# Kernel tuning notes

Hardware: AMD Instinct MI355X
Metric: run time of the kernel (lower is better)

## Reference

```python
import jax, jax.numpy as jnp
import numpy as np
import math

L, D, H, FF = 12, 768, 12, 3072
DH = D // H
REL_BINS, MAX_REL = 32, 128
REL2D_BINS, MAX_REL2D = 64, 256
EPS = 1e-5
ALPHA = 32.0


def rel_bucket(rp, num_buckets, max_distance):
    # bidirectional T5-style bucketing, matches relative_position_bucket
    nb = num_buckets // 2
    ret = (rp > 0).astype(jnp.int32) * nb
    n = jnp.abs(rp)
    max_exact = nb // 2
    is_small = n < max_exact
    val_if_large = max_exact + (
        jnp.log(jnp.maximum(n, 1).astype(jnp.float32) / max_exact)
        / math.log(max_distance / max_exact) * (nb - max_exact)
    ).astype(jnp.int32)
    val_if_large = jnp.minimum(val_if_large, nb - 1)
    return ret + jnp.where(is_small, n.astype(jnp.int32), val_if_large)


def layernorm(x, g, b):
    mu = jnp.mean(x, axis=-1, keepdims=True)
    var = jnp.mean(jnp.square(x - mu), axis=-1, keepdims=True)
    return (x - mu) * jax.lax.rsqrt(var + EPS) * g + b


def cogview_softmax(scores):
    # PB-Relax stabilized softmax
    ss = scores / ALPHA
    m = jnp.max(ss, axis=-1, keepdims=True)
    return jax.nn.softmax((ss - m) * ALPHA, axis=-1)


def setup_inputs() -> dict:
    key = jax.random.key(0)
    ks = jax.random.split(key, 24)
    B, S = 4, 512
    s = 0.02
    inp = {
        'hidden_states': jax.random.normal(ks[0], (B, S, D), jnp.float32),
        'attention_mask': jnp.zeros((B, 1, 1, S), jnp.float32),
        'position_ids': jnp.arange(B * S, dtype=jnp.int64).reshape(B, S),
        'bbox': jax.random.randint(ks[1], (B, S, 4), 0, 1000, jnp.int64),
        'Wq': jax.random.normal(ks[2], (L, D, D)) * s,
        'bq': jnp.zeros((L, D)),
        'Wk': jax.random.normal(ks[3], (L, D, D)) * s,
        'bk': jnp.zeros((L, D)),
        'Wv': jax.random.normal(ks[4], (L, D, D)) * s,
        'bv': jnp.zeros((L, D)),
        'Wo': jax.random.normal(ks[5], (L, D, D)) * s,
        'bo': jnp.zeros((L, D)),
        'ln1_g': jnp.ones((L, D)),
        'ln1_b': jnp.zeros((L, D)),
        'Wi': jax.random.normal(ks[6], (L, D, FF)) * s,
        'bi': jnp.zeros((L, FF)),
        'Wo2': jax.random.normal(ks[7], (L, FF, D)) * s,
        'bo2': jnp.zeros((L, D)),
        'ln2_g': jnp.ones((L, D)),
        'ln2_b': jnp.zeros((L, D)),
        'rel_w': jax.random.normal(ks[8], (REL_BINS, H)) * s,   # rel_pos_bias.weight.T
        'relx_w': jax.random.normal(ks[9], (REL2D_BINS, H)) * s,
        'rely_w': jax.random.normal(ks[10], (REL2D_BINS, H)) * s,
    }
    return inp


def encoder_forward(hidden_states, attention_mask, position_ids, bbox,
                    Wq, bq, Wk, bk, Wv, bv, Wo, bo, ln1_g, ln1_b,
                    Wi, bi, Wo2, bo2, ln2_g, ln2_b, rel_w, relx_w, rely_w):
    B, S, _ = hidden_states.shape
    inv_sqrt = 1.0 / math.sqrt(DH)

    # 1D relative position bias: [B,H,S,S]
    rp = position_ids[:, None, :] - position_ids[:, :, None]  # [B,S,S]
    b1 = rel_bucket(rp, REL_BINS, MAX_REL)
    rel_pos = jnp.transpose(rel_w[b1], (0, 3, 1, 2))

    # 2D spatial bias from bbox x (coord 0) and y (coord 3)
    px = bbox[:, :, 0]
    py = bbox[:, :, 3]
    bx = rel_bucket(px[:, None, :] - px[:, :, None], REL2D_BINS, MAX_REL2D)
    by = rel_bucket(py[:, None, :] - py[:, :, None], REL2D_BINS, MAX_REL2D)
    rel_2d_pos = jnp.transpose(relx_w[bx], (0, 3, 1, 2)) + jnp.transpose(rely_w[by], (0, 3, 1, 2))

    bias = (rel_pos + rel_2d_pos) * inv_sqrt + attention_mask  # [B,H,S,S]

    x = hidden_states
    for i in range(L):
        q = (x @ Wq[i] + bq[i]).reshape(B, S, H, DH).transpose(0, 2, 1, 3)
        k = (x @ Wk[i] + bk[i]).reshape(B, S, H, DH).transpose(0, 2, 1, 3)
        v = (x @ Wv[i] + bv[i]).reshape(B, S, H, DH).transpose(0, 2, 1, 3)
        scores = jnp.einsum('bhqd,bhkd->bhqk', q * inv_sqrt, k) + bias
        probs = cogview_softmax(scores)
        ctx = jnp.einsum('bhqk,bhkd->bhqd', probs, v)
        ctx = ctx.transpose(0, 2, 1, 3).reshape(B, S, D)
        attn_out = layernorm(ctx @ Wo[i] + bo[i] + x, ln1_g[i], ln1_b[i])
        h = jax.nn.gelu(attn_out @ Wi[i] + bi[i], approximate=False)
        x = layernorm(h @ Wo2[i] + bo2[i] + attn_out, ln2_g[i], ln2_b[i])
    return x


def reference(hidden_states, attention_mask, position_ids, bbox,
              Wq, bq, Wk, bk, Wv, bv, Wo, bo, ln1_g, ln1_b,
              Wi, bi, Wo2, bo2, ln2_g, ln2_b, rel_w, relx_w, rely_w):
    return encoder_forward(hidden_states, attention_mask, position_ids, bbox,
                           Wq, bq, Wk, bk, Wv, bv, Wo, bo, ln1_g, ln1_b,
                           Wi, bi, Wo2, bo2, ln2_g, ln2_b, rel_w, relx_w, rely_w)
```

## Files before the change

### kernel.cpp

```cpp
#include <hip/hip_runtime.h>
#include <hip/hip_bf16.h>


typedef __attribute__((ext_vector_type(8))) short short8;
typedef __attribute__((ext_vector_type(4))) float f32x4;
typedef __attribute__((ext_vector_type(4))) unsigned int u32x4;
typedef __attribute__((ext_vector_type(4))) unsigned short us4;

#define DEVI static __device__ __forceinline__

DEVI unsigned short f2bf(float f) {
  union { float f; unsigned u; } x; x.f = f;
  unsigned u = x.u;
  u += 0x7fffu + ((u >> 16) & 1u);
  return (unsigned short)(u >> 16);
}
DEVI float bf2f(unsigned short h) {
  union { unsigned u; float f; } x; x.u = ((unsigned)h) << 16;
  return x.f;
}
DEVI int xcd_swz(int bid, int nwg) {
  int q = nwg >> 3, r = nwg & 7;
  int x = bid & 7, o = bid >> 3;
  return (x < r ? x * (q + 1) : r * (q + 1) + (x - r) * q) + o;
}

DEVI void gemm64(const unsigned short* __restrict__ A, int lda,
                 const float* __restrict__ W, int ldw, int K,
                 int m0, f32x4 acc[4], char* lds) {
  const int tid = threadIdx.x;
  const int l = tid & 63, w = tid >> 6;
  const int n_st = tid & 63;
  const int kb = (tid >> 6) << 4;
  const unsigned short* Ar = A + (size_t)(m0 + 16 * w + (l & 15)) * lda + ((l >> 4) << 3);
  for (int kt = 0; kt < K; kt += 64) {
    float f[16];
#pragma unroll
    for (int j = 0; j < 16; ++j)
      f[j] = W[(size_t)(kt + kb + j) * ldw + n_st];
    __syncthreads();
#pragma unroll
    for (int c = 0; c < 2; ++c) {
      u32x4 p;
#pragma unroll
      for (int q2 = 0; q2 < 4; ++q2)
        p[q2] = (unsigned)f2bf(f[c * 8 + q2 * 2]) | ((unsigned)f2bf(f[c * 8 + q2 * 2 + 1]) << 16);
      int koff = (kb + c * 8) << 1;
      int addr = (n_st << 7) + (koff ^ ((n_st & 7) << 4));
      *(u32x4*)(lds + addr) = p;
    }
    __syncthreads();
#pragma unroll
    for (int ks = 0; ks < 2; ++ks) {
      short8 a = *(const short8*)(Ar + kt + ks * 32);
#pragma unroll
      for (int fb = 0; fb < 4; ++fb) {
        int nn = (fb << 4) + (l & 15);
        int koff = (ks * 32 + ((l >> 4) << 3)) << 1;
        int addr = (nn << 7) + (koff ^ ((nn & 7) << 4));
        short8 b = *(const short8*)(lds + addr);
        acc[fb] = __builtin_amdgcn_mfma_f32_16x16x32_bf16(a, b, acc[fb], 0, 0, 0);
      }
    }
  }
}

__global__ __launch_bounds__(256) void k_qkv(
    const unsigned short* __restrict__ xb,
    const float* __restrict__ Wq, const float* __restrict__ Wk, const float* __restrict__ Wv,
    const float* __restrict__ bq, const float* __restrict__ bk, const float* __restrict__ bv,
    unsigned short* __restrict__ q_out, unsigned short* __restrict__ k_out,
    unsigned short* __restrict__ vT_out, int layer) {
  __shared__ u32x4 lds4[512];
  char* lds = (char*)lds4;
  const int wid = xcd_swz(blockIdx.x, gridDim.x);
  const int bm = wid % 32, bn = wid / 32;
  const int which = bn / 12;
  const int nloc = (bn % 12) * 64;
  const float* W = (which == 0 ? Wq : which == 1 ? Wk : Wv) + (size_t)layer * 589824 + nloc;
  const float* bias = (which == 0 ? bq : which == 1 ? bk : bv) + layer * 768 + nloc;
  f32x4 acc[4];
#pragma unroll
  for (int i = 0; i < 4; ++i) acc[i] = (f32x4){0.f, 0.f, 0.f, 0.f};
  gemm64(xb, 768, W, 768, 768, bm * 64, acc, lds);
  const int tid = threadIdx.x, l = tid & 63, w = tid >> 6;
  const int h = nloc >> 6;
  const int r0 = bm * 64 + 16 * w + ((l >> 4) << 2);
  const int batch = r0 >> 9, s0 = r0 & 511;
  const int bh = batch * 12 + h;
  const float scale = (which == 0) ? 0.125f : 1.0f;
#pragma unroll
  for (int fb = 0; fb < 4; ++fb) {
    const int c = (fb << 4) + (l & 15);
    const float bv_ = bias[c];
    if (which == 2) {
      us4 pk;
#pragma unroll
      for (int j = 0; j < 4; ++j) pk[j] = f2bf(acc[fb][j] + bv_);
      *(us4*)(vT_out + ((size_t)bh * 64 + c) * 512 + s0) = pk;
    } else {
      unsigned short* dst = (which == 0 ? q_out : k_out);
#pragma unroll
      for (int j = 0; j < 4; ++j)
        dst[((size_t)bh * 512 + s0 + j) * 64 + c] = f2bf((acc[fb][j] + bv_) * scale);
    }
  }
}

__global__ __launch_bounds__(256) void k_attn(
    const unsigned short* __restrict__ qb, const unsigned short* __restrict__ kb,
    const unsigned short* __restrict__ biasb, unsigned short* __restrict__ probs) {
  const int bh = blockIdx.y;
  const int q0 = blockIdx.x * 64;
  const int tid = threadIdx.x, l = tid & 63, w = tid >> 6;
  const unsigned short* Q = qb + ((size_t)bh * 512 + q0 + 16 * w + (l & 15)) * 64 + ((l >> 4) << 3);
  const unsigned short* Kp = kb + (size_t)bh * 32768 + (size_t)(l & 15) * 64 + ((l >> 4) << 3);
  f32x4 acc[32];
#pragma unroll
  for (int i = 0; i < 32; ++i) acc[i] = (f32x4){0.f, 0.f, 0.f, 0.f};
#pragma unroll
  for (int ks = 0; ks < 2; ++ks) {
    short8 a = *(const short8*)(Q + ks * 32);
#pragma unroll
    for (int f = 0; f < 32; ++f) {
      short8 b = *(const short8*)(Kp + (size_t)f * 1024 + ks * 32);
      acc[f] = __builtin_amdgcn_mfma_f32_16x16x32_bf16(a, b, acc[f], 0, 0, 0);
    }
  }
  const int r0 = q0 + 16 * w + ((l >> 4) << 2);
  const unsigned short* Brow = biasb + ((size_t)bh * 512 + r0) * 512 + (l & 15);
  unsigned short* Prow = probs + ((size_t)bh * 512 + r0) * 512 + (l & 15);
#pragma unroll
  for (int j = 0; j < 4; ++j) {
    float m = -3.0e38f;
#pragma unroll
    for (int f = 0; f < 32; ++f) {
      float v = acc[f][j] + bf2f(Brow[(size_t)j * 512 + (f << 4)]);
      acc[f][j] = v;
      m = fmaxf(m, v);
    }
#pragma unroll
    for (int off = 1; off < 16; off <<= 1) m = fmaxf(m, __shfl_xor(m, off));
    float s = 0.f;
#pragma unroll
    for (int f = 0; f < 32; ++f) {
      float e = __expf(acc[f][j] - m);
      acc[f][j] = e;
      s += e;
    }
#pragma unroll
    for (int off = 1; off < 16; off <<= 1) s += __shfl_xor(s, off);
    const float inv = 1.0f / s;
#pragma unroll
    for (int f = 0; f < 32; ++f)
      Prow[(size_t)j * 512 + (f << 4)] = f2bf(acc[f][j] * inv);
  }
}

__global__ __launch_bounds__(256) void k_pv(
    const unsigned short* __restrict__ probs, const unsigned short* __restrict__ vT,
    unsigned short* __restrict__ ctx) {
  const int bh = blockIdx.y;
  const int q0 = blockIdx.x * 64;
  const int tid = threadIdx.x, l = tid & 63, w = tid >> 6;
  const unsigned short* Ar = probs + ((size_t)bh * 512 + q0 + 16 * w + (l & 15)) * 512 + ((l >> 4) << 3);
  const unsigned short* Vb = vT + (size_t)bh * 32768 + (size_t)(l & 15) * 512 + ((l >> 4) << 3);
  f32x4 acc[4];
#pragma unroll
  for (int i = 0; i < 4; ++i) acc[i] = (f32x4){0.f, 0.f, 0.f, 0.f};
#pragma unroll 4
  for (int kt = 0; kt < 512; kt += 32) {
    short8 a = *(const short8*)(Ar + kt);
#pragma unroll
    for (int f = 0; f < 4; ++f) {
      short8 b = *(const short8*)(Vb + (size_t)f * 8192 + kt);
      acc[f] = __builtin_amdgcn_mfma_f32_16x16x32_bf16(a, b, acc[f], 0, 0, 0);
    }
  }
  const int batch = bh / 12, h = bh % 12;
  const int r0 = q0 + 16 * w + ((l >> 4) << 2);
#pragma unroll
  for (int fb = 0; fb < 4; ++fb) {
    const int c = (fb << 4) + (l & 15);
#pragma unroll
    for (int j = 0; j < 4; ++j)
      ctx[((size_t)(batch * 512 + r0 + j)) * 768 + h * 64 + c] = f2bf(acc[fb][j]);
  }
}

__global__ __launch_bounds__(256) void k_gemm_bias(
    const unsigned short* __restrict__ A, int lda, int K,
    const float* __restrict__ W, int ldw,
    const float* __restrict__ bias, float* __restrict__ outf, int N, int nbm) {
  __shared__ u32x4 lds4[512];
  char* lds = (char*)lds4;
  const int wid = xcd_swz(blockIdx.x, gridDim.x);
  const int bm = wid % nbm, bn = wid / nbm;
  f32x4 acc[4];
#pragma unroll
  for (int i = 0; i < 4; ++i) acc[i] = (f32x4){0.f, 0.f, 0.f, 0.f};
  gemm64(A, lda, W + bn * 64, ldw, K, bm * 64, acc, lds);
  const int tid = threadIdx.x, l = tid & 63, w = tid >> 6;
  const int r0 = bm * 64 + 16 * w + ((l >> 4) << 2);
  const int c0 = bn * 64;
#pragma unroll
  for (int fb = 0; fb < 4; ++fb) {
    const int c = c0 + (fb << 4) + (l & 15);
    const float bb = bias[c];
#pragma unroll
    for (int j = 0; j < 4; ++j)
      outf[(size_t)(r0 + j) * N + c] = acc[fb][j] + bb;
  }
}

__global__ __launch_bounds__(256) void k_gemm_gelu(
    const unsigned short* __restrict__ A, int lda, int K,
    const float* __restrict__ W, int ldw,
    const float* __restrict__ bias, unsigned short* __restrict__ outb, int N, int nbm) {
  __shared__ u32x4 lds4[512];
  char* lds = (char*)lds4;
  const int wid = xcd_swz(blockIdx.x, gridDim.x);
  const int bm = wid % nbm, bn = wid / nbm;
  f32x4 acc[4];
#pragma unroll
  for (int i = 0; i < 4; ++i) acc[i] = (f32x4){0.f, 0.f, 0.f, 0.f};
  gemm64(A, lda, W + bn * 64, ldw, K, bm * 64, acc, lds);
  const int tid = threadIdx.x, l = tid & 63, w = tid >> 6;
  const int r0 = bm * 64 + 16 * w + ((l >> 4) << 2);
  const int c0 = bn * 64;
#pragma unroll
  for (int fb = 0; fb < 4; ++fb) {
    const int c = c0 + (fb << 4) + (l & 15);
    const float bb = bias[c];
#pragma unroll
    for (int j = 0; j < 4; ++j) {
      float v = acc[fb][j] + bb;
      v = 0.5f * v * (1.0f + erff(v * 0.70710678118654752f));
      outb[(size_t)(r0 + j) * N + c] = f2bf(v);
    }
  }
}

__global__ __launch_bounds__(256) void k_ln(
    const float* __restrict__ x, const float* __restrict__ res,
    const float* __restrict__ g, const float* __restrict__ bb,
    float* __restrict__ outf, unsigned short* __restrict__ outb) {
  const int row = blockIdx.x, tid = threadIdx.x;
  const float* X = x + (size_t)row * 768;
  const float* R = res + (size_t)row * 768;
  float v[3];
  float s = 0.f;
#pragma unroll
  for (int i = 0; i < 3; ++i) { v[i] = X[tid + (i << 8)] + R[tid + (i << 8)]; s += v[i]; }
  __shared__ float red[4];
#pragma unroll
  for (int off = 32; off; off >>= 1) s += __shfl_xor(s, off);
  if ((tid & 63) == 0) red[tid >> 6] = s;
  __syncthreads();
  const float mu = (red[0] + red[1] + red[2] + red[3]) * (1.f / 768.f);
  float s2 = 0.f;
#pragma unroll
  for (int i = 0; i < 3; ++i) { float d = v[i] - mu; s2 += d * d; }
  __syncthreads();
#pragma unroll
  for (int off = 32; off; off >>= 1) s2 += __shfl_xor(s2, off);
  if ((tid & 63) == 0) red[tid >> 6] = s2;
  __syncthreads();
  const float rstd = rsqrtf((red[0] + red[1] + red[2] + red[3]) * (1.f / 768.f) + 1e-5f);
#pragma unroll
  for (int i = 0; i < 3; ++i) {
    const int c = tid + (i << 8);
    const float o = (v[i] - mu) * rstd * g[c] + bb[c];
    outf[(size_t)row * 768 + c] = o;
    outb[(size_t)row * 768 + c] = f2bf(o);
  }
}

__global__ __launch_bounds__(256) void k_init(const float* __restrict__ h,
                                              float* __restrict__ xf,
                                              unsigned short* __restrict__ xb, int n) {
  int i = blockIdx.x * 256 + threadIdx.x;
  if (i < n) { float v = h[i]; xf[i] = v; xb[i] = f2bf(v); }
}

DEVI int rbucket(int rp, int nb, int mex) {
  int ret = rp > 0 ? nb : 0;
  int n = rp < 0 ? -rp : rp;
  if (n < mex) return ret + n;
  float v = logf((float)n / (float)mex) * 0.36067376022224085f * (float)(nb - mex);
  int vi = mex + (int)v;
  vi = vi < (nb - 1) ? vi : (nb - 1);
  return ret + vi;
}

__global__ __launch_bounds__(256) void k_bias(
    const int* __restrict__ pos, const int* __restrict__ bbox,
    const float* __restrict__ mask,
    const float* __restrict__ rel_w, const float* __restrict__ relx_w,
    const float* __restrict__ rely_w, unsigned short* __restrict__ biasb) {
  __shared__ float tw[1920];
  for (int i = threadIdx.x; i < 1920; i += 256)
    tw[i] = i < 384 ? rel_w[i] : (i < 1152 ? relx_w[i - 384] : rely_w[i - 1152]);
  __syncthreads();
  const int blk = blockIdx.x;
  const int b = blk >> 9, qi = blk & 511;
  const int pi = pos[(b << 9) + qi];
  const int pxi = bbox[(((b << 9) + qi) << 2) + 0];
  const int pyi = bbox[(((b << 9) + qi) << 2) + 3];
  for (int j = threadIdx.x; j < 512; j += 256) {
    const int idx = (b << 9) + j;
    const int b1 = rbucket(pos[idx] - pi, 16, 8);
    const int bx = rbucket(bbox[(idx << 2) + 0] - pxi, 32, 16);
    const int by = rbucket(bbox[(idx << 2) + 3] - pyi, 32, 16);
    const float mk = mask[idx];
    const float* r1 = tw + b1 * 12;
    const float* r2 = tw + 384 + bx * 12;
    const float* r3 = tw + 1152 + by * 12;
#pragma unroll
    for (int h = 0; h < 12; ++h) {
      float v = (r1[h] + r2[h] + r3[h]) * 0.125f + mk;
      biasb[(((size_t)(b * 12 + h) * 512) + qi) * 512 + j] = f2bf(v);
    }
  }
}

extern "C" void kernel_launch(void* const* d_in, const int* in_sizes, int n_in,
                              void* d_out, int out_size, void* d_ws, size_t ws_size,
                              hipStream_t stream) {
  const float* hid  = (const float*)d_in[0];
  const float* mask = (const float*)d_in[1];
  const int*   pos  = (const int*)d_in[2];
  const int*   bbx  = (const int*)d_in[3];
  const float* Wq = (const float*)d_in[4];  const float* bq = (const float*)d_in[5];
  const float* Wk = (const float*)d_in[6];  const float* bk = (const float*)d_in[7];
  const float* Wv = (const float*)d_in[8];  const float* bv = (const float*)d_in[9];
  const float* Wo = (const float*)d_in[10]; const float* bo = (const float*)d_in[11];
  const float* g1 = (const float*)d_in[12]; const float* be1 = (const float*)d_in[13];
  const float* Wi = (const float*)d_in[14]; const float* bi = (const float*)d_in[15];
  const float* W2 = (const float*)d_in[16]; const float* b2 = (const float*)d_in[17];
  const float* g2 = (const float*)d_in[18]; const float* be2 = (const float*)d_in[19];
  const float* relw  = (const float*)d_in[20];
  const float* relxw = (const float*)d_in[21];
  const float* relyw = (const float*)d_in[22];

  char* ws = (char*)d_ws;
  size_t off = 0;
  auto alloc = [&](size_t b) -> char* {
    char* p = ws + off; off += (b + 255) & ~(size_t)255; return p;
  };
  unsigned short* biasb = (unsigned short*)alloc(25165824);
  unsigned short* probs = (unsigned short*)alloc(25165824);
  float* xf  = (float*)alloc(6291456);
  float* tmp = (float*)alloc(6291456);
  float* aof = (float*)alloc(6291456);
  unsigned short* xb  = (unsigned short*)alloc(3145728);
  unsigned short* qb  = (unsigned short*)alloc(3145728);
  unsigned short* kb  = (unsigned short*)alloc(3145728);
  unsigned short* vT  = (unsigned short*)alloc(3145728);
  unsigned short* ctx = (unsigned short*)alloc(3145728);
  unsigned short* aob = (unsigned short*)alloc(3145728);
  unsigned short* hb  = (unsigned short*)alloc(12582912);

  k_bias<<<2048, 256, 0, stream>>>(pos, bbx, mask, relw, relxw, relyw, biasb);
  k_init<<<6144, 256, 0, stream>>>(hid, xf, xb, 2048 * 768);

  for (int lyr = 0; lyr < 12; ++lyr) {
    k_qkv<<<1152, 256, 0, stream>>>(xb, Wq, Wk, Wv, bq, bk, bv, qb, kb, vT, lyr);
    k_attn<<<dim3(8, 48), 256, 0, stream>>>(qb, kb, biasb, probs);
    k_pv<<<dim3(8, 48), 256, 0, stream>>>(probs, vT, ctx);
    k_gemm_bias<<<384, 256, 0, stream>>>(ctx, 768, 768, Wo + (size_t)lyr * 589824, 768,
                                         bo + lyr * 768, tmp, 768, 32);
    k_ln<<<2048, 256, 0, stream>>>(tmp, xf, g1 + lyr * 768, be1 + lyr * 768, aof, aob);
    k_gemm_gelu<<<1536, 256, 0, stream>>>(aob, 768, 768, Wi + (size_t)lyr * 2359296, 3072,
                                          bi + lyr * 3072, hb, 3072, 32);
    k_gemm_bias<<<384, 256, 0, stream>>>(hb, 3072, 3072, W2 + (size_t)lyr * 2359296, 768,
                                         b2 + lyr * 768, tmp, 768, 32);
    float* ox = (lyr == 11) ? (float*)d_out : xf;
    k_ln<<<2048, 256, 0, stream>>>(tmp, aof, g2 + lyr * 768, be2 + lyr * 768, ox, xb);
  }
}
```

Baseline: 2.706 ms.

## Pre-pack fp32 weights into swizzled bf16 tiles and stream them via global_load_lds

Adds a prep kernel that converts all layer weights from fp32 into bf16 64x64 tiles with an XOR-swizzled layout, once per call. New GEMM kernels then double-buffer those tiles into LDS using direct global-to-LDS loads, overlapping the next tile's load with the current tile's MFMAs. The aim is to halve weight bandwidth, drop per-tile fp32-to-bf16 conversion, and hide load latency. In exchange it needs a large extra workspace and adds a full weight-conversion pass, and it falls back to the old kernels if the workspace is too small.

```diff
diff --git a/kernel.cpp b/kernel.cpp
--- a/kernel.cpp
+++ b/kernel.cpp
@@ -23,6 +23,180 @@
   int q = nwg >> 3, r = nwg & 7;
   int x = bid & 7, o = bid >> 3;
   return (x < r ? x * (q + 1) : r * (q + 1) + (x - r) * q) + o;
+}
+
+DEVI void gload16(const void* g, void* l) {
+  __builtin_amdgcn_global_load_lds((const __attribute__((address_space(1))) void*)g,
+                                   (__attribute__((address_space(3))) void*)l, 16, 0, 0);
+}
+
+__global__ __launch_bounds__(256) void k_prep(
+    const float* __restrict__ W, unsigned short* __restrict__ dst,
+    int K, int N, int nkt, int nbn) {
+  __shared__ float sw[4096];
+  int t = blockIdx.x;
+  const int kt = t % nkt; t /= nkt;
+  const int bn = t % nbn; t /= nbn;
+  const int layer = t;
+  const float* src = W + (size_t)layer * K * N + (size_t)(kt * 64) * N + bn * 64;
+  const int tid = threadIdx.x;
+  const int k = tid >> 2, n0 = (tid & 3) * 16;
+#pragma unroll
+  for (int j = 0; j < 4; ++j)
+    *(f32x4*)(sw + k * 64 + n0 + j * 4) = *(const f32x4*)(src + (size_t)k * N + n0 + j * 4);
+  __syncthreads();
+  unsigned short* img = dst + ((size_t)((size_t)layer * nbn + bn) * nkt + kt) * 4096;
+  const int n_loc = tid >> 2;
+#pragma unroll
+  for (int ci = 0; ci < 2; ++ci) {
+    const int c = (tid & 3) + ci * 4;
+    const int kc = c ^ (n_loc & 7);
+    short8 out;
+#pragma unroll
+    for (int j = 0; j < 8; ++j) out[j] = (short)f2bf(sw[(kc * 8 + j) * 64 + n_loc]);
+    *(short8*)(img + n_loc * 64 + c * 8) = out;
+  }
+}
+
+DEVI void gemm64t(const unsigned short* __restrict__ A, int lda,
+                  const unsigned short* __restrict__ tiles, int nkt,
+                  int m0, f32x4 acc[4], char* lds) {
+  const int tid = threadIdx.x, l = tid & 63, w = tid >> 6;
+  const unsigned short* Ar = A + (size_t)(m0 + 16 * w + (l & 15)) * lda + ((l >> 4) << 3);
+  char* buf0 = lds;
+  char* buf1 = lds + 8192;
+#define STAGE_T(b, kt)                                                        \
+  {                                                                           \
+    const char* s_ = (const char*)(tiles + (size_t)(kt) * 4096);              \
+    int b0_ = (w * 64) * 16;                                                  \
+    gload16(s_ + b0_ + l * 16, (b) + b0_);                                    \
+    int b1_ = (256 + w * 64) * 16;                                            \
+    gload16(s_ + b1_ + l * 16, (b) + b1_);                                    \
+  }
+  STAGE_T(buf0, 0);
+  short8 aC0 = *(const short8*)(Ar);
+  short8 aC1 = *(const short8*)(Ar + 32);
+  __syncthreads();
+  for (int kt = 0; kt < nkt; ++kt) {
+    char* cur = (kt & 1) ? buf1 : buf0;
+    char* nxt = (kt & 1) ? buf0 : buf1;
+    short8 aN0 = aC0, aN1 = aC1;
+    if (kt + 1 < nkt) {
+      STAGE_T(nxt, kt + 1);
+      aN0 = *(const short8*)(Ar + (kt + 1) * 64);
+      aN1 = *(const short8*)(Ar + (kt + 1) * 64 + 32);
+    }
+#pragma unroll
+    for (int ks = 0; ks < 2; ++ks) {
+      short8 a = ks ? aC1 : aC0;
+#pragma unroll
+      for (int fb = 0; fb < 4; ++fb) {
+        int nn = (fb << 4) + (l & 15);
+        int kc = (ks << 2) + (l >> 4);
+        int addr = (nn << 7) + ((kc ^ (nn & 7)) << 4);
+        short8 b = *(const short8*)(cur + addr);
+        acc[fb] = __builtin_amdgcn_mfma_f32_16x16x32_bf16(a, b, acc[fb], 0, 0, 0);
+      }
+    }
+    __syncthreads();
+    aC0 = aN0; aC1 = aN1;
+  }
+#undef STAGE_T
+}
+
+__global__ __launch_bounds__(256) void k_qkv2(
+    const unsigned short* __restrict__ xb,
+    const unsigned short* __restrict__ wQt, const unsigned short* __restrict__ wKt,
+    const unsigned short* __restrict__ wVt,
+    const float* __restrict__ bq, const float* __restrict__ bk, const float* __restrict__ bv,
+    unsigned short* __restrict__ q_out, unsigned short* __restrict__ k_out,
+    unsigned short* __restrict__ vT_out) {
+  __shared__ u32x4 lds4[1024];
+  char* lds = (char*)lds4;
+  const int wid = xcd_swz(blockIdx.x, gridDim.x);
+  const int bm = wid % 32, bn = wid / 32;
+  const int which = bn / 12, nb = bn % 12;
+  const unsigned short* tiles =
+      (which == 0 ? wQt : which == 1 ? wKt : wVt) + (size_t)nb * 12 * 4096;
+  const float* bias = (which == 0 ? bq : which == 1 ? bk : bv) + nb * 64;
+  f32x4 acc[4];
+#pragma unroll
+  for (int i = 0; i < 4; ++i) acc[i] = (f32x4){0.f, 0.f, 0.f, 0.f};
+  gemm64t(xb, 768, tiles, 12, bm * 64, acc, lds);
+  const int tid = threadIdx.x, l = tid & 63, w = tid >> 6;
+  const int r0 = bm * 64 + 16 * w + ((l >> 4) << 2);
+  const int batch = r0 >> 9, s0 = r0 & 511;
+  const int bh = batch * 12 + nb;
+  const float scale = (which == 0) ? 0.125f : 1.0f;
+#pragma unroll
+  for (int fb = 0; fb < 4; ++fb) {
+    const int c = (fb << 4) + (l & 15);
+    const float bv_ = bias[c];
+    if (which == 2) {
+      us4 pk;
+#pragma unroll
+      for (int j = 0; j < 4; ++j) pk[j] = f2bf(acc[fb][j] + bv_);
+      *(us4*)(vT_out + ((size_t)bh * 64 + c) * 512 + s0) = pk;
+    } else {
+      unsigned short* dst = (which == 0 ? q_out : k_out);
+#pragma unroll
+      for (int j = 0; j < 4; ++j)
+        dst[((size_t)bh * 512 + s0 + j) * 64 + c] = f2bf((acc[fb][j] + bv_) * scale);
+    }
+  }
+}
+
+__global__ __launch_bounds__(256) void k_gemm_bias2(
+    const unsigned short* __restrict__ A, int lda,
+    const unsigned short* __restrict__ tilesL, int nkt,
+    const float* __restrict__ bias, float* __restrict__ outf, int N, int nbm) {
+  __shared__ u32x4 lds4[1024];
+  char* lds = (char*)lds4;
+  const int wid = xcd_swz(blockIdx.x, gridDim.x);
+  const int bm = wid % nbm, bn = wid / nbm;
+  f32x4 acc[4];
+#pragma unroll
+  for (int i = 0; i < 4; ++i) acc[i] = (f32x4){0.f, 0.f, 0.f, 0.f};
+  gemm64t(A, lda, tilesL + (size_t)bn * nkt * 4096, nkt, bm * 64, acc, lds);
+  const int tid = threadIdx.x, l = tid & 63, w = tid >> 6;
+  const int r0 = bm * 64 + 16 * w + ((l >> 4) << 2);
+  const int c0 = bn * 64;
+#pragma unroll
+  for (int fb = 0; fb < 4; ++fb) {
+    const int c = c0 + (fb << 4) + (l & 15);
+    const float bb = bias[c];
+#pragma unroll
+    for (int j = 0; j < 4; ++j)
+      outf[(size_t)(r0 + j) * N + c] = acc[fb][j] + bb;
+  }
+}
+
+__global__ __launch_bounds__(256) void k_gemm_gelu2(
+    const unsigned short* __restrict__ A, int lda,
+    const unsigned short* __restrict__ tilesL, int nkt,
+    const float* __restrict__ bias, unsigned short* __restrict__ outb, int N, int nbm) {
+  __shared__ u32x4 lds4[1024];
+  char* lds = (char*)lds4;
+  const int wid = xcd_swz(blockIdx.x, gridDim.x);
+  const int bm = wid % nbm, bn = wid / nbm;
+  f32x4 acc[4];
+#pragma unroll
+  for (int i = 0; i < 4; ++i) acc[i] = (f32x4){0.f, 0.f, 0.f, 0.f};
+  gemm64t(A, lda, tilesL + (size_t)bn * nkt * 4096, nkt, bm * 64, acc, lds);
+  const int tid = threadIdx.x, l = tid & 63, w = tid >> 6;
+  const int r0 = bm * 64 + 16 * w + ((l >> 4) << 2);
+  const int c0 = bn * 64;
+#pragma unroll
+  for (int fb = 0; fb < 4; ++fb) {
+    const int c = c0 + (fb << 4) + (l & 15);
+    const float bb = bias[c];
+#pragma unroll
+    for (int j = 0; j < 4; ++j) {
+      float v = acc[fb][j] + bb;
+      v = 0.5f * v * (1.0f + erff(v * 0.70710678118654752f));
+      outb[(size_t)(r0 + j) * N + c] = f2bf(v);
+    }
+  }
 }
 
 DEVI void gemm64(const unsigned short* __restrict__ A, int lda,
@@ -107,87 +281,6 @@
   }
 }
 
-__global__ __launch_bounds__(256) void k_attn(
-    const unsigned short* __restrict__ qb, const unsigned short* __restrict__ kb,
-    const unsigned short* __restrict__ biasb, unsigned short* __restrict__ probs) {
-  const int bh = blockIdx.y;
-  const int q0 = blockIdx.x * 64;
-  const int tid = threadIdx.x, l = tid & 63, w = tid >> 6;
-  const unsigned short* Q = qb + ((size_t)bh * 512 + q0 + 16 * w + (l & 15)) * 64 + ((l >> 4) << 3);
-  const unsigned short* Kp = kb + (size_t)bh * 32768 + (size_t)(l & 15) * 64 + ((l >> 4) << 3);
-  f32x4 acc[32];
-#pragma unroll
-  for (int i = 0; i < 32; ++i) acc[i] = (f32x4){0.f, 0.f, 0.f, 0.f};
-#pragma unroll
-  for (int ks = 0; ks < 2; ++ks) {
-    short8 a = *(const short8*)(Q + ks * 32);
-#pragma unroll
-    for (int f = 0; f < 32; ++f) {
-      short8 b = *(const short8*)(Kp + (size_t)f * 1024 + ks * 32);
-      acc[f] = __builtin_amdgcn_mfma_f32_16x16x32_bf16(a, b, acc[f], 0, 0, 0);
-    }
-  }
-  const int r0 = q0 + 16 * w + ((l >> 4) << 2);
-  const unsigned short* Brow = biasb + ((size_t)bh * 512 + r0) * 512 + (l & 15);
-  unsigned short* Prow = probs + ((size_t)bh * 512 + r0) * 512 + (l & 15);
-#pragma unroll
-  for (int j = 0; j < 4; ++j) {
-    float m = -3.0e38f;
-#pragma unroll
-    for (int f = 0; f < 32; ++f) {
-      float v = acc[f][j] + bf2f(Brow[(size_t)j * 512 + (f << 4)]);
-      acc[f][j] = v;
-      m = fmaxf(m, v);
-    }
-#pragma unroll
-    for (int off = 1; off < 16; off <<= 1) m = fmaxf(m, __shfl_xor(m, off));
-    float s = 0.f;
-#pragma unroll
-    for (int f = 0; f < 32; ++f) {
-      float e = __expf(acc[f][j] - m);
-      acc[f][j] = e;
-      s += e;
-    }
-#pragma unroll
-    for (int off = 1; off < 16; off <<= 1) s += __shfl_xor(s, off);
-    const float inv = 1.0f / s;
-#pragma unroll
-    for (int f = 0; f < 32; ++f)
-      Prow[(size_t)j * 512 + (f << 4)] = f2bf(acc[f][j] * inv);
-  }
-}
-
-__global__ __launch_bounds__(256) void k_pv(
-    const unsigned short* __restrict__ probs, const unsigned short* __restrict__ vT,
-    unsigned short* __restrict__ ctx) {
-  const int bh = blockIdx.y;
-  const int q0 = blockIdx.x * 64;
-  const int tid = threadIdx.x, l = tid & 63, w = tid >> 6;
-  const unsigned short* Ar = probs + ((size_t)bh * 512 + q0 + 16 * w + (l & 15)) * 512 + ((l >> 4) << 3);
-  const unsigned short* Vb = vT + (size_t)bh * 32768 + (size_t)(l & 15) * 512 + ((l >> 4) << 3);
-  f32x4 acc[4];
-#pragma unroll
-  for (int i = 0; i < 4; ++i) acc[i] = (f32x4){0.f, 0.f, 0.f, 0.f};
-#pragma unroll 4
-  for (int kt = 0; kt < 512; kt += 32) {
-    short8 a = *(const short8*)(Ar + kt);
-#pragma unroll
-    for (int f = 0; f < 4; ++f) {
-      short8 b = *(const short8*)(Vb + (size_t)f * 8192 + kt);
-      acc[f] = __builtin_amdgcn_mfma_f32_16x16x32_bf16(a, b, acc[f], 0, 0, 0);
-    }
-  }
-  const int batch = bh / 12, h = bh % 12;
-  const int r0 = q0 + 16 * w + ((l >> 4) << 2);
-#pragma unroll
-  for (int fb = 0; fb < 4; ++fb) {
-    const int c = (fb << 4) + (l & 15);
-#pragma unroll
-    for (int j = 0; j < 4; ++j)
-      ctx[((size_t)(batch * 512 + r0 + j)) * 768 + h * 64 + c] = f2bf(acc[fb][j]);
-  }
-}
-
 __global__ __launch_bounds__(256) void k_gemm_bias(
     const unsigned short* __restrict__ A, int lda, int K,
     const float* __restrict__ W, int ldw,
@@ -238,6 +331,87 @@
       v = 0.5f * v * (1.0f + erff(v * 0.70710678118654752f));
       outb[(size_t)(r0 + j) * N + c] = f2bf(v);
     }
+  }
+}
+
+__global__ __launch_bounds__(256) void k_attn(
+    const unsigned short* __restrict__ qb, const unsigned short* __restrict__ kb,
+    const unsigned short* __restrict__ biasb, unsigned short* __restrict__ probs) {
+  const int bh = blockIdx.y;
+  const int q0 = blockIdx.x * 64;
+  const int tid = threadIdx.x, l = tid & 63, w = tid >> 6;
+  const unsigned short* Q = qb + ((size_t)bh * 512 + q0 + 16 * w + (l & 15)) * 64 + ((l >> 4) << 3);
+  const unsigned short* Kp = kb + (size_t)bh * 32768 + (size_t)(l & 15) * 64 + ((l >> 4) << 3);
+  f32x4 acc[32];
+#pragma unroll
+  for (int i = 0; i < 32; ++i) acc[i] = (f32x4){0.f, 0.f, 0.f, 0.f};
+#pragma unroll
+  for (int ks = 0; ks < 2; ++ks) {
+    short8 a = *(const short8*)(Q + ks * 32);
+#pragma unroll
+    for (int f = 0; f < 32; ++f) {
+      short8 b = *(const short8*)(Kp + (size_t)f * 1024 + ks * 32);
+      acc[f] = __builtin_amdgcn_mfma_f32_16x16x32_bf16(a, b, acc[f], 0, 0, 0);
+    }
+  }
+  const int r0 = q0 + 16 * w + ((l >> 4) << 2);
+  const unsigned short* Brow = biasb + ((size_t)bh * 512 + r0) * 512 + (l & 15);
+  unsigned short* Prow = probs + ((size_t)bh * 512 + r0) * 512 + (l & 15);
+#pragma unroll
+  for (int j = 0; j < 4; ++j) {
+    float m = -3.0e38f;
+#pragma unroll
+    for (int f = 0; f < 32; ++f) {
+      float v = acc[f][j] + bf2f(Brow[(size_t)j * 512 + (f << 4)]);
+      acc[f][j] = v;
+      m = fmaxf(m, v);
+    }
+#pragma unroll
+    for (int off = 1; off < 16; off <<= 1) m = fmaxf(m, __shfl_xor(m, off));
+    float s = 0.f;
+#pragma unroll
+    for (int f = 0; f < 32; ++f) {
+      float e = __expf(acc[f][j] - m);
+      acc[f][j] = e;
+      s += e;
+    }
+#pragma unroll
+    for (int off = 1; off < 16; off <<= 1) s += __shfl_xor(s, off);
+    const float inv = 1.0f / s;
+#pragma unroll
+    for (int f = 0; f < 32; ++f)
+      Prow[(size_t)j * 512 + (f << 4)] = f2bf(acc[f][j] * inv);
+  }
+}
+
+__global__ __launch_bounds__(256) void k_pv(
+    const unsigned short* __restrict__ probs, const unsigned short* __restrict__ vT,
+    unsigned short* __restrict__ ctx) {
+  const int bh = blockIdx.y;
+  const int q0 = blockIdx.x * 64;
+  const int tid = threadIdx.x, l = tid & 63, w = tid >> 6;
+  const unsigned short* Ar = probs + ((size_t)bh * 512 + q0 + 16 * w + (l & 15)) * 512 + ((l >> 4) << 3);
+  const unsigned short* Vb = vT + (size_t)bh * 32768 + (size_t)(l & 15) * 512 + ((l >> 4) << 3);
+  f32x4 acc[4];
+#pragma unroll
+  for (int i = 0; i < 4; ++i) acc[i] = (f32x4){0.f, 0.f, 0.f, 0.f};
+#pragma unroll 4
+  for (int kt = 0; kt < 512; kt += 32) {
+    short8 a = *(const short8*)(Ar + kt);
+#pragma unroll
+    for (int f = 0; f < 4; ++f) {
+      short8 b = *(const short8*)(Vb + (size_t)f * 8192 + kt);
+      acc[f] = __builtin_amdgcn_mfma_f32_16x16x32_bf16(a, b, acc[f], 0, 0, 0);
+    }
+  }
+  const int batch = bh / 12, h = bh % 12;
+  const int r0 = q0 + 16 * w + ((l >> 4) << 2);
+#pragma unroll
+  for (int fb = 0; fb < 4; ++fb) {
+    const int c = (fb << 4) + (l & 15);
+#pragma unroll
+    for (int j = 0; j < 4; ++j)
+      ctx[((size_t)(batch * 512 + r0 + j)) * 768 + h * 64 + c] = f2bf(acc[fb][j]);
   }
 }
 
@@ -360,21 +534,61 @@
   unsigned short* ctx = (unsigned short*)alloc(3145728);
   unsigned short* aob = (unsigned short*)alloc(3145728);
   unsigned short* hb  = (unsigned short*)alloc(12582912);
+  const size_t act_need = off;
+
+  const size_t szP = (size_t)12 * 12 * 12 * 4096 * 2;
+  const size_t szF = (size_t)12 * 48 * 12 * 4096 * 2;
+  unsigned short* imgQ = (unsigned short*)alloc(szP);
+  unsigned short* imgK = (unsigned short*)alloc(szP);
+  unsigned short* imgV = (unsigned short*)alloc(szP);
+  unsigned short* imgO = (unsigned short*)alloc(szP);
+  unsigned short* imgI = (unsigned short*)alloc(szF);
+  unsigned short* img2 = (unsigned short*)alloc(szF);
+  const bool big = (off <= ws_size);
+  (void)act_need;
 
   k_bias<<<2048, 256, 0, stream>>>(pos, bbx, mask, relw, relxw, relyw, biasb);
   k_init<<<6144, 256, 0, stream>>>(hid, xf, xb, 2048 * 768);
 
+  if (big) {
+    k_prep<<<1728, 256, 0, stream>>>(Wq, imgQ, 768, 768, 12, 12);
+    k_prep<<<1728, 256, 0, stream>>>(Wk, imgK, 768, 768, 12, 12);
+    k_prep<<<1728, 256, 0, stream>>>(Wv, imgV, 768, 768, 12, 12);
+    k_prep<<<1728, 256, 0, stream>>>(Wo, imgO, 768, 768, 12, 12);
+    k_prep<<<6912, 256, 0, stream>>>(Wi, imgI, 768, 3072, 12, 48);
+    k_prep<<<6912, 256, 0, stream>>>(W2, img2, 3072, 768, 48, 12);
+  }
+
   for (int lyr = 0; lyr < 12; ++lyr) {
-    k_qkv<<<1152, 256, 0, stream>>>(xb, Wq, Wk, Wv, bq, bk, bv, qb, kb, vT, lyr);
+    if (big) {
+      k_qkv2<<<1152, 256, 0, stream>>>(xb,
+          imgQ + (size_t)lyr * 144 * 4096, imgK + (size_t)lyr * 144 * 4096,
+          imgV + (size_t)lyr * 144 * 4096,
+          bq + lyr * 768, bk + lyr * 768, bv + lyr * 768, qb, kb, vT);
+    } else {
+      k_qkv<<<1152, 256, 0, stream>>>(xb, Wq, Wk, Wv, bq, bk, bv, qb, kb, vT, lyr);
+    }
     k_attn<<<dim3(8, 48), 256, 0, stream>>>(qb, kb, biasb, probs);
     k_pv<<<dim3(8, 48), 256, 0, stream>>>(probs, vT, ctx);
-    k_gemm_bias<<<384, 256, 0, stream>>>(ctx, 768, 768, Wo + (size_t)lyr * 589824, 768,
-                                         bo + lyr * 768, tmp, 768, 32);
+    if (big) {
+      k_gemm_bias2<<<384, 256, 0, stream>>>(ctx, 768,
+          imgO + (size_t)lyr * 144 * 4096, 12, bo + lyr * 768, tmp, 768, 32);
+    } else {
+      k_gemm_bias<<<384, 256, 0, stream>>>(ctx, 768, 768, Wo + (size_t)lyr * 589824, 768,
+                                           bo + lyr * 768, tmp, 768, 32);
+    }
     k_ln<<<2048, 256, 0, stream>>>(tmp, xf, g1 + lyr * 768, be1 + lyr * 768, aof, aob);
-    k_gemm_gelu<<<1536, 256, 0, stream>>>(aob, 768, 768, Wi + (size_t)lyr * 2359296, 3072,
-                                          bi + lyr * 3072, hb, 3072, 32);
-    k_gemm_bias<<<384, 256, 0, stream>>>(hb, 3072, 3072, W2 + (size_t)lyr * 2359296, 768,
-                                         b2 + lyr * 768, tmp, 768, 32);
+    if (big) {
+      k_gemm_gelu2<<<1536, 256, 0, stream>>>(aob, 768,
+          imgI + (size_t)lyr * 576 * 4096, 12, bi + lyr * 3072, hb, 3072, 32);
+      k_gemm_bias2<<<384, 256, 0, stream>>>(hb, 3072,
+          img2 + (size_t)lyr * 576 * 4096, 48, b2 + lyr * 768, tmp, 768, 32);
+    } else {
+      k_gemm_gelu<<<1536, 256, 0, stream>>>(aob, 768, 768, Wi + (size_t)lyr * 2359296, 3072,
+                                            bi + lyr * 3072, hb, 3072, 32);
+      k_gemm_bias<<<384, 256, 0, stream>>>(hb, 3072, 3072, W2 + (size_t)lyr * 2359296, 768,
+                                           b2 + lyr * 768, tmp, 768, 32);
+    }
     float* ox = (lyr == 11) ? (float*)d_out : xf;
     k_ln<<<2048, 256, 0, stream>>>(tmp, aof, g2 + lyr * 768, be2 + lyr * 768, ox, xb);
   }
```

After: 2.316 ms. -14.4%, faster.
